# Kernel tuning notes

Measured on AMD Instinct MI355X. Metric: run time of the kernel, lower is better.

The kernel has to match this reference:

```python
import jax, jax.numpy as jnp
import numpy as np
import math

NUM_HEADS = 16
ROPE_BASE = 10000.0

def _rotate_half(t):
    d = t.shape[-1]
    x1, x2 = t[..., : d // 2], t[..., d // 2 :]
    return jnp.concatenate([-x2, x1], axis=-1)

def _rope_tables(seq_len, head_dim, dtype):
    inv_freq = 1.0 / (ROPE_BASE ** (jnp.arange(0, head_dim, 2, dtype=jnp.float32) / head_dim))
    t = jnp.arange(seq_len, dtype=jnp.float32)
    freqs = jnp.einsum('i,j->ij', t, inv_freq)          # [S, d/2]
    emb = jnp.concatenate([freqs, freqs], axis=-1)      # [S, d]
    return jnp.cos(emb).astype(dtype), jnp.sin(emb).astype(dtype)

def setup_inputs() -> dict:
    key = jax.random.key(0)
    ks = jax.random.split(key, 6)
    B, S, HID = 4, 2048, 1024
    x = jax.random.normal(ks[0], (B, S, HID), dtype=jnp.float32)
    w_scale = 0.02
    Wq = jax.random.normal(ks[1], (HID, HID), dtype=jnp.float32) * w_scale
    Wk = jax.random.normal(ks[2], (HID, HID), dtype=jnp.float32) * w_scale
    Wv = jax.random.normal(ks[3], (HID, HID), dtype=jnp.float32) * w_scale
    Wo = jax.random.normal(ks[4], (HID, HID), dtype=jnp.float32) * w_scale
    # ragged valid lengths in [S//2, S] so each sequence is non-trivial
    seq_lens = jax.random.randint(ks[5], (B,), S // 2, S + 1, dtype=jnp.int32)
    return {"x": x, "Wq": Wq, "Wk": Wk, "Wv": Wv, "Wo": Wo, "seq_lens": seq_lens}

def reference(x, Wq, Wk, Wv, Wo, seq_lens):
    B, S, HID = x.shape
    H = NUM_HEADS
    d = HID // H
    scale = 1.0 / math.sqrt(d)

    # qkv projections (nn.Linear, no bias)
    q = (x @ Wq).reshape(B, S, H, d)
    k = (x @ Wk).reshape(B, S, H, d)
    v = (x @ Wv).reshape(B, S, H, d)

    # fused RoPE, positions start at 0 for every sequence (prefill, beg=0)
    cos, sin = _rope_tables(S, d, x.dtype)              # [S, d]
    cos = cos[None, :, None, :]
    sin = sin[None, :, None, :]
    q = q * cos + _rotate_half(q) * sin
    k = k * cos + _rotate_half(k) * sin

    # causal SDPA over ragged batch via padding masks
    scores = jnp.einsum('bqhd,bkhd->bhqk', q, k) * scale  # [B,H,S,S]
    pos = jnp.arange(S)
    causal = pos[:, None] >= pos[None, :]                 # [S,S]
    valid_k = pos[None, :] < seq_lens[:, None]            # [B,S]
    mask = causal[None, None, :, :] & valid_k[:, None, None, :]
    neg = jnp.asarray(-1e9, dtype=scores.dtype)
    attn = jax.nn.softmax(jnp.where(mask, scores, neg), axis=-1)
    out = jnp.einsum('bhqk,bkhd->bqhd', attn, v).reshape(B, S, HID)

    out = out @ Wo
    # zero out padded query positions (they do not exist in CatTensor)
    valid_q = (pos[None, :] < seq_lens[:, None])[..., None]
    return jnp.where(valid_q, out, jnp.zeros((), dtype=out.dtype))
```

## Files before the change

### kernel.cpp

```cpp
#include <hip/hip_runtime.h>
#include <hip/hip_bf16.h>

typedef __attribute__((ext_vector_type(8))) short short8;
typedef __attribute__((ext_vector_type(4))) float f32x4;

constexpr int Bc   = 4;
constexpr int Sc   = 2048;
constexpr int HIDc = 1024;
constexpr int Hc   = 16;
constexpr size_t FB = (size_t)Bc * Sc * HIDc;
constexpr size_t WN = (size_t)HIDc * HIDc;
constexpr size_t TB = (size_t)Sc * 32;

__device__ __forceinline__ int get_L(const int* seq, int b)
{
    return (seq[1] == 0) ? seq[2 * b] : seq[b];
}

__device__ __forceinline__ short f2bf(float v)
{
    __hip_bfloat16 h = __float2bfloat16(v);
    return *reinterpret_cast<short*>(&h);
}
__device__ __forceinline__ float bf2f(short s)
{
    __hip_bfloat16 h = *reinterpret_cast<__hip_bfloat16*>(&s);
    return __bfloat162float(h);
}
__device__ __forceinline__ unsigned pack2(short a, short b)
{
    return (unsigned)(unsigned short)a | ((unsigned)(unsigned short)b << 16);
}

__global__ __launch_bounds__(256) void rope_tab(float* __restrict__ ct,
                                                float* __restrict__ st)
{
    const int idx = blockIdx.x * 256 + threadIdx.x;
    const int s = idx >> 5;
    const int j = idx & 31;
    const float ang = (float)s * powf(10000.0f, -(float)j * (1.0f / 32.0f));
    ct[idx] = cosf(ang);
    st[idx] = sinf(ang);
}

__global__ __launch_bounds__(256) void split_pass(const float* __restrict__ in,
                                                  short* __restrict__ hi,
                                                  short* __restrict__ lo)
{
    const size_t i8 = ((size_t)blockIdx.x * 256 + threadIdx.x) * 8;
    const float4 u0 = *(const float4*)(in + i8);
    const float4 u1 = *(const float4*)(in + i8 + 4);
    const float v[8] = {u0.x, u0.y, u0.z, u0.w, u1.x, u1.y, u1.z, u1.w};
    short8 h, l;
#pragma unroll
    for (int j = 0; j < 8; j++) {
        const short hb = f2bf(v[j]);
        h[j] = hb;
        l[j] = f2bf(v[j] - bf2f(hb));
    }
    *(short8*)(hi + i8) = h;
    *(short8*)(lo + i8) = l;
}

__global__ __launch_bounds__(256) void rope_split(const float* __restrict__ p,
                                                  short* __restrict__ hi,
                                                  short* __restrict__ lo)
{
    const int idx = blockIdx.x * 256 + threadIdx.x;
    const int jc = idx & 3;
    const int h  = (idx >> 2) & 15;
    const int s  = (idx >> 6) & 2047;
    const int b  = idx >> 17;
    const int j0 = jc * 8;
    const size_t base = ((size_t)(b * Sc + s)) * HIDc + h * 64 + j0;

    const float4 a0 = *(const float4*)(p + base);
    const float4 a1 = *(const float4*)(p + base + 4);
    const float4 b0 = *(const float4*)(p + base + 32);
    const float4 b1 = *(const float4*)(p + base + 36);
    const float x1[8] = {a0.x, a0.y, a0.z, a0.w, a1.x, a1.y, a1.z, a1.w};
    const float x2[8] = {b0.x, b0.y, b0.z, b0.w, b1.x, b1.y, b1.z, b1.w};

    short8 h1, h2, l1, l2;
#pragma unroll
    for (int jj = 0; jj < 8; jj++) {
        const int j = j0 + jj;
        const float ang = (float)s * powf(10000.0f, -(float)j * (1.0f / 32.0f));
        const float cv = cosf(ang);
        const float sv = sinf(ang);
        const float y1 = x1[jj] * cv - x2[jj] * sv;
        const float y2 = x2[jj] * cv + x1[jj] * sv;
        const short hb1 = f2bf(y1), hb2 = f2bf(y2);
        h1[jj] = hb1; l1[jj] = f2bf(y1 - bf2f(hb1));
        h2[jj] = hb2; l2[jj] = f2bf(y2 - bf2f(hb2));
    }
    *(short8*)(hi + base)      = h1;
    *(short8*)(hi + base + 32) = h2;
    *(short8*)(lo + base)      = l1;
    *(short8*)(lo + base + 32) = l2;
}

__global__ __launch_bounds__(256) void vsplit_t(const float* __restrict__ V,
                                                short* __restrict__ th,
                                                short* __restrict__ tl)
{
    __shared__ float T[64][65];
    const int s0 = blockIdx.x * 64;
    const int h  = blockIdx.y & 15;
    const int b  = blockIdx.y >> 4;
    const int t  = threadIdx.x;
    const int r  = t >> 2;
    const int c  = (t & 3) * 16;
#pragma unroll
    for (int j = 0; j < 4; j++) {
        const float4 u = *(const float4*)(V + ((size_t)(b * Sc + s0 + r)) * HIDc + h * 64 + c + j * 4);
        T[r][c + j * 4 + 0] = u.x; T[r][c + j * 4 + 1] = u.y;
        T[r][c + j * 4 + 2] = u.z; T[r][c + j * 4 + 3] = u.w;
    }
    __syncthreads();
    short8 h0, h1, l0, l1;
#pragma unroll
    for (int j = 0; j < 8; j++) {
        const float v = T[c + j][r];
        const short hb = f2bf(v);
        h0[j] = hb; l0[j] = f2bf(v - bf2f(hb));
    }
#pragma unroll
    for (int j = 0; j < 8; j++) {
        const float v = T[c + 8 + j][r];
        const short hb = f2bf(v);
        h1[j] = hb; l1[j] = f2bf(v - bf2f(hb));
    }
    const size_t dst = ((size_t)(b * Hc + h) * 64 + r) * Sc + s0 + c;
    *(short8*)(th + dst)     = h0;
    *(short8*)(th + dst + 8) = h1;
    *(short8*)(tl + dst)     = l0;
    *(short8*)(tl + dst + 8) = l1;
}

__device__ __forceinline__ void wsplit_body(const float* __restrict__ W,
                                            short* __restrict__ th,
                                            short* __restrict__ tl,
                                            float (*T)[65])
{
    const int t  = threadIdx.x;
    const int n0 = blockIdx.x * 64;
    const int k0 = blockIdx.y * 64;
    const int r  = t >> 2;
    const int c  = (t & 3) * 16;
#pragma unroll
    for (int j = 0; j < 4; j++) {
        const float4 u = *(const float4*)(W + (size_t)(k0 + r) * HIDc + n0 + c + j * 4);
        T[r][c + j * 4 + 0] = u.x; T[r][c + j * 4 + 1] = u.y;
        T[r][c + j * 4 + 2] = u.z; T[r][c + j * 4 + 3] = u.w;
    }
    __syncthreads();
    short8 h0, h1, l0, l1;
#pragma unroll
    for (int j = 0; j < 8; j++) {
        const float v = T[c + j][r];
        const short hb = f2bf(v);
        h0[j] = hb; l0[j] = f2bf(v - bf2f(hb));
    }
#pragma unroll
    for (int j = 0; j < 8; j++) {
        const float v = T[c + 8 + j][r];
        const short hb = f2bf(v);
        h1[j] = hb; l1[j] = f2bf(v - bf2f(hb));
    }
    const size_t dst = (size_t)(n0 + r) * HIDc + k0 + c;
    *(short8*)(th + dst)     = h0;
    *(short8*)(th + dst + 8) = h1;
    *(short8*)(tl + dst)     = l0;
    *(short8*)(tl + dst + 8) = l1;
}

__global__ __launch_bounds__(256) void wsplit_t(const float* __restrict__ W,
                                                short* __restrict__ th,
                                                short* __restrict__ tl)
{
    __shared__ float T[64][65];
    wsplit_body(W, th, tl, T);
}

__global__ __launch_bounds__(256) void wsplit4_t(
    const float* __restrict__ W0, const float* __restrict__ W1,
    const float* __restrict__ W2, const float* __restrict__ W3,
    short* __restrict__ out)
{
    __shared__ float T[64][65];
    const int z = blockIdx.z;
    const float* W = (z == 0) ? W0 : (z == 1) ? W1 : (z == 2) ? W2 : W3;
    short* th = out + (size_t)z * 2 * WN;
    wsplit_body(W, th, th + WN, T);
}

__device__ __forceinline__ void gemm_x3_acc(
    const short* __restrict__ Ah, const short* __restrict__ Al,
    const short* __restrict__ Bh, const short* __restrict__ Bl,
    const int m0, const int n0,
    short* AhS, short* AlS, short* BhS, short* BlS,
    f32x4 (&acc)[4][4])
{
    const int t    = threadIdx.x;
    const int lane = t & 63;
    const int wid  = t >> 6;
    const int wr   = (wid >> 1) * 64;
    const int wc   = (wid & 1) * 64;
    const int lr   = lane & 15;
    const int lg   = lane >> 4;

#pragma unroll
    for (int mi = 0; mi < 4; mi++)
#pragma unroll
        for (int ni = 0; ni < 4; ni++) acc[mi][ni] = (f32x4)(0.f);

    for (int k0 = 0; k0 < HIDc; k0 += 64) {
        __syncthreads();
#pragma unroll
        for (int i = 0; i < 4; i++) {
            const int o  = i * 4096 + t * 16;
            const int r  = o >> 7;
            const int sc = (o & 127) ^ ((r & 7) << 4);
            const int k  = sc >> 1;
            const size_t ga = (size_t)(m0 + r) * HIDc + k0 + k;
            const size_t gb = (size_t)(n0 + r) * HIDc + k0 + k;
            __builtin_amdgcn_global_load_lds(
                (const __attribute__((address_space(1))) void*)(Ah + ga),
                (__attribute__((address_space(3))) void*)(AhS + (o >> 1)), 16, 0, 0);
            __builtin_amdgcn_global_load_lds(
                (const __attribute__((address_space(1))) void*)(Al + ga),
                (__attribute__((address_space(3))) void*)(AlS + (o >> 1)), 16, 0, 0);
            __builtin_amdgcn_global_load_lds(
                (const __attribute__((address_space(1))) void*)(Bh + gb),
                (__attribute__((address_space(3))) void*)(BhS + (o >> 1)), 16, 0, 0);
            __builtin_amdgcn_global_load_lds(
                (const __attribute__((address_space(1))) void*)(Bl + gb),
                (__attribute__((address_space(3))) void*)(BlS + (o >> 1)), 16, 0, 0);
        }
        __syncthreads();

        short8 a_h[4][2], a_l[4][2];
#pragma unroll
        for (int mi = 0; mi < 4; mi++) {
            const int r = wr + mi * 16 + lr;
#pragma unroll
            for (int kk = 0; kk < 2; kk++) {
                const int cb  = kk * 64 + lg * 16;
                const int off = r * 128 + (cb ^ ((r & 7) << 4));
                a_h[mi][kk] = *(const short8*)((const char*)AhS + off);
                a_l[mi][kk] = *(const short8*)((const char*)AlS + off);
            }
        }
#pragma unroll
        for (int ni = 0; ni < 4; ni++) {
            const int rn = wc + ni * 16 + lr;
            short8 b_h[2], b_l[2];
#pragma unroll
            for (int kk = 0; kk < 2; kk++) {
                const int cb  = kk * 64 + lg * 16;
                const int off = rn * 128 + (cb ^ ((rn & 7) << 4));
                b_h[kk] = *(const short8*)((const char*)BhS + off);
                b_l[kk] = *(const short8*)((const char*)BlS + off);
            }
#pragma unroll
            for (int mi = 0; mi < 4; mi++) {
#pragma unroll
                for (int kk = 0; kk < 2; kk++) {
                    acc[mi][ni] = __builtin_amdgcn_mfma_f32_16x16x32_bf16(
                        a_h[mi][kk], b_h[kk], acc[mi][ni], 0, 0, 0);
                    acc[mi][ni] = __builtin_amdgcn_mfma_f32_16x16x32_bf16(
                        a_h[mi][kk], b_l[kk], acc[mi][ni], 0, 0, 0);
                    acc[mi][ni] = __builtin_amdgcn_mfma_f32_16x16x32_bf16(
                        a_l[mi][kk], b_h[kk], acc[mi][ni], 0, 0, 0);
                }
            }
        }
    }
}

__global__ __launch_bounds__(256, 2) void gemm_x3(
    const short* __restrict__ Ah, const short* __restrict__ Al,
    const short* __restrict__ Bh, const short* __restrict__ Bl,
    float* __restrict__ C, const int* __restrict__ seq)
{
    __shared__ alignas(16) short AhS[128 * 64];
    __shared__ alignas(16) short AlS[128 * 64];
    __shared__ alignas(16) short BhS[128 * 64];
    __shared__ alignas(16) short BlS[128 * 64];
    const int F   = blockIdx.x + 8 * blockIdx.y;
    const int xcd = F & 7;
    const int s   = F >> 3;
    const int ly  = xcd + 8 * (s >> 3);
    const int lx  = s & 7;
    const int m0 = ly * 128, n0 = lx * 128;

    f32x4 acc[4][4];
    gemm_x3_acc(Ah, Al, Bh, Bl, m0, n0, AhS, AlS, BhS, BlS, acc);

    const int lane = threadIdx.x & 63;
    const int wid  = threadIdx.x >> 6;
    const int wr   = (wid >> 1) * 64;
    const int wc   = (wid & 1) * 64;
    const int lr   = lane & 15;
    const int lg   = lane >> 4;
#pragma unroll
    for (int mi = 0; mi < 4; mi++) {
#pragma unroll
        for (int rr = 0; rr < 4; rr++) {
            const int row = m0 + wr + mi * 16 + lg * 4 + rr;
            bool zero = false;
            if (seq != nullptr) zero = ((row & 2047) >= get_L(seq, row >> 11));
#pragma unroll
            for (int ni = 0; ni < 4; ni++) {
                const float v = zero ? 0.f : acc[mi][ni][rr];
                C[(size_t)row * HIDc + n0 + wc + ni * 16 + lr] = v;
            }
        }
    }
}

__global__ __launch_bounds__(256, 2) void gemm_x3_qkv_rope(
    const short* __restrict__ Ah, const short* __restrict__ Al,
    const short* __restrict__ Wbase, short* __restrict__ outS,
    float* __restrict__ outF,
    const float* __restrict__ cos_t, const float* __restrict__ sin_t)
{
    __shared__ alignas(16) short AhS[128 * 64];
    __shared__ alignas(16) short AlS[128 * 64];
    __shared__ alignas(16) short BhS[128 * 64];
    __shared__ alignas(16) short BlS[128 * 64];
    const int F   = blockIdx.x + 8 * blockIdx.y + 512 * blockIdx.z;
    const int xcd = F & 7;
    const int s   = F >> 3;
    const int ly  = xcd + 8 * (s / 24);
    const int rem = s % 24;
    const int lx  = rem & 7;
    const int lz  = rem >> 3;
    const int m0 = ly * 128, n0 = lx * 128;
    const short* Bh = Wbase + (size_t)lz * 2 * WN;

    f32x4 acc[4][4];
    gemm_x3_acc(Ah, Al, Bh, Bh + WN, m0, n0, AhS, AlS, BhS, BlS, acc);

    const int lane = threadIdx.x & 63;
    const int wid  = threadIdx.x >> 6;
    const int wr   = (wid >> 1) * 64;
    const int wc   = (wid & 1) * 64;
    const int lr   = lane & 15;
    const int lg   = lane >> 4;

    if (lz < 2) {
        short* Ch = outS + (size_t)lz * 2 * FB;
        short* Cl = Ch + FB;
#pragma unroll
        for (int mi = 0; mi < 4; mi++) {
#pragma unroll
            for (int rr = 0; rr < 4; rr++) {
                const int row = m0 + wr + mi * 16 + lg * 4 + rr;
                const int sp  = row & 2047;
                const float c0  = cos_t[sp * 32 + lr];
                const float sn0 = sin_t[sp * 32 + lr];
                const float c1  = cos_t[sp * 32 + 16 + lr];
                const float sn1 = sin_t[sp * 32 + 16 + lr];
                const float x0 = acc[mi][0][rr];
                const float x1 = acc[mi][1][rr];
                const float x2 = acc[mi][2][rr];
                const float x3 = acc[mi][3][rr];
                const float y[4] = {x0 * c0 - x2 * sn0,
                                    x1 * c1 - x3 * sn1,
                                    x2 * c0 + x0 * sn0,
                                    x3 * c1 + x1 * sn1};
                const size_t cb = (size_t)row * HIDc + n0 + wc + lr;
#pragma unroll
                for (int ni = 0; ni < 4; ni++) {
                    const short hb = f2bf(y[ni]);
                    Ch[cb + ni * 16] = hb;
                    Cl[cb + ni * 16] = f2bf(y[ni] - bf2f(hb));
                }
            }
        }
    } else {
#pragma unroll
        for (int mi = 0; mi < 4; mi++) {
#pragma unroll
            for (int rr = 0; rr < 4; rr++) {
                const int row = m0 + wr + mi * 16 + lg * 4 + rr;
#pragma unroll
                for (int ni = 0; ni < 4; ni++)
                    outF[(size_t)row * HIDc + n0 + wc + ni * 16 + lr] = acc[mi][ni][rr];
            }
        }
    }
}

__global__ __launch_bounds__(256, 3) void attn_mfma_sw(
    const short* __restrict__ Qh, const short* __restrict__ Ql,
    const short* __restrict__ Kh, const short* __restrict__ Kl,
    const short* __restrict__ Vth, const short* __restrict__ Vtl,
    short* __restrict__ Oh, short* __restrict__ Ol,
    const int* __restrict__ seq)
{
    __shared__ alignas(16) short KhS[64 * 64];
    __shared__ alignas(16) short KlS[64 * 64];
    __shared__ alignas(16) short VhS[64 * 64];
    __shared__ alignas(16) short VlS[64 * 64];
    __shared__ alignas(16) short PhS[4][16 * 64];
    __shared__ alignas(16) short PlS[4][16 * 64];

    const int blk  = blockIdx.x;
    const int bh   = blk & 63;
    const int qt   = 31 - (blk >> 6);
    const int h    = bh & 15;
    const int b    = bh >> 4;
    const int q0   = qt * 64;
    const int L    = get_L(seq, b);
    const int t    = threadIdx.x;
    const int w    = t >> 6;
    const int lane = t & 63;
    const int lr   = lane & 15;
    const int lg   = lane >> 4;

    if (q0 >= L) {
        const int r = t >> 2;
        const int c = (t & 3) * 16;
        const size_t base = ((size_t)(b * Sc + q0 + r)) * HIDc + h * 64 + c;
        const short8 z = {0, 0, 0, 0, 0, 0, 0, 0};
        *(short8*)(Oh + base)     = z;
        *(short8*)(Oh + base + 8) = z;
        *(short8*)(Ol + base)     = z;
        *(short8*)(Ol + base + 8) = z;
        return;
    }

    short8 qb_h[2], qb_l[2];
    {
        const size_t qrow = ((size_t)(b * Sc + q0 + w * 16 + lr)) * HIDc + h * 64;
        qb_h[0] = *(const short8*)(Qh + qrow + lg * 8);
        qb_h[1] = *(const short8*)(Qh + qrow + 32 + lg * 8);
        qb_l[0] = *(const short8*)(Ql + qrow + lg * 8);
        qb_l[1] = *(const short8*)(Ql + qrow + 32 + lg * 8);
    }

    f32x4 oacc[4];
#pragma unroll
    for (int t2 = 0; t2 < 4; t2++) oacc[t2] = (f32x4)(0.f);
    float m_s = -1.0e30f, l_s = 0.f;

    const int qpos = q0 + w * 16 + lr;

    const int kend = min(q0 + 64, L);
    for (int kb = 0; kb < kend; kb += 64) {
        __syncthreads();
#pragma unroll
        for (int i = 0; i < 2; i++) {
            const int o  = i * 4096 + t * 16;
            const int r  = o >> 7;
            const int sc = (o & 127) ^ ((r & 7) << 4);
            const int k  = sc >> 1;
            const size_t gk = ((size_t)(b * Sc + kb + r)) * HIDc + h * 64 + k;
            const size_t gv = ((size_t)(b * Hc + h) * 64 + r) * Sc + kb + k;
            __builtin_amdgcn_global_load_lds(
                (const __attribute__((address_space(1))) void*)(Kh + gk),
                (__attribute__((address_space(3))) void*)((char*)KhS + o), 16, 0, 0);
            __builtin_amdgcn_global_load_lds(
                (const __attribute__((address_space(1))) void*)(Kl + gk),
                (__attribute__((address_space(3))) void*)((char*)KlS + o), 16, 0, 0);
            __builtin_amdgcn_global_load_lds(
                (const __attribute__((address_space(1))) void*)(Vth + gv),
                (__attribute__((address_space(3))) void*)((char*)VhS + o), 16, 0, 0);
            __builtin_amdgcn_global_load_lds(
                (const __attribute__((address_space(1))) void*)(Vtl + gv),
                (__attribute__((address_space(3))) void*)((char*)VlS + o), 16, 0, 0);
        }
        __syncthreads();

        f32x4 s4[4];
#pragma unroll
        for (int tt = 0; tt < 4; tt++) s4[tt] = (f32x4)(0.f);
        __builtin_amdgcn_s_setprio(1);
#pragma unroll
        for (int tt = 0; tt < 4; tt++) {
            const int rn = tt * 16 + lr;
#pragma unroll
            for (int kk = 0; kk < 2; kk++) {
                const int off = rn * 128 + ((kk * 64 + lg * 16) ^ ((rn & 7) << 4));
                const short8 ka_h = *(const short8*)((const char*)KhS + off);
                const short8 ka_l = *(const short8*)((const char*)KlS + off);
                s4[tt] = __builtin_amdgcn_mfma_f32_16x16x32_bf16(ka_h, qb_h[kk], s4[tt], 0, 0, 0);
                s4[tt] = __builtin_amdgcn_mfma_f32_16x16x32_bf16(ka_h, qb_l[kk], s4[tt], 0, 0, 0);
                s4[tt] = __builtin_amdgcn_mfma_f32_16x16x32_bf16(ka_l, qb_h[kk], s4[tt], 0, 0, 0);
            }
        }
        __builtin_amdgcn_s_setprio(0);

        float tmax = -1.0e30f;
#pragma unroll
        for (int tt = 0; tt < 4; tt++)
#pragma unroll
            for (int r = 0; r < 4; r++) {
                const int kpos = kb + tt * 16 + lg * 4 + r;
                const bool valid = (kpos <= qpos) && (kpos < L);
                const float v = valid ? s4[tt][r] * 0.125f : -1.0e9f;
                s4[tt][r] = v;
                tmax = fmaxf(tmax, v);
            }
        tmax = fmaxf(tmax, __shfl_xor(tmax, 16));
        tmax = fmaxf(tmax, __shfl_xor(tmax, 32));
        const float mnew  = fmaxf(m_s, tmax);
        const float alpha = __expf(m_s - mnew);
        float psum = 0.f;
#pragma unroll
        for (int tt = 0; tt < 4; tt++)
#pragma unroll
            for (int r = 0; r < 4; r++) {
                const float e = __expf(s4[tt][r] - mnew);
                s4[tt][r] = e;
                psum += e;
            }
        psum += __shfl_xor(psum, 16);
        psum += __shfl_xor(psum, 32);
        l_s = alpha * l_s + psum;
        m_s = mnew;

#pragma unroll
        for (int r = 0; r < 4; r++) {
            const float ar = __shfl(alpha, lg * 4 + r);
#pragma unroll
            for (int t2 = 0; t2 < 4; t2++) oacc[t2][r] *= ar;
        }

#pragma unroll
        for (int tt = 0; tt < 4; tt++) {
            const short h0 = f2bf(s4[tt][0]); const short l0 = f2bf(s4[tt][0] - bf2f(h0));
            const short h1 = f2bf(s4[tt][1]); const short l1 = f2bf(s4[tt][1] - bf2f(h1));
            const short h2 = f2bf(s4[tt][2]); const short l2 = f2bf(s4[tt][2] - bf2f(h2));
            const short h3 = f2bf(s4[tt][3]); const short l3 = f2bf(s4[tt][3] - bf2f(h3));
            const int off = lr * 128 + ((tt * 32 + lg * 8) ^ ((lr & 7) << 4));
            uint2 uh; uh.x = pack2(h0, h1); uh.y = pack2(h2, h3);
            uint2 ul; ul.x = pack2(l0, l1); ul.y = pack2(l2, l3);
            *(uint2*)((char*)&PhS[w][0] + off) = uh;
            *(uint2*)((char*)&PlS[w][0] + off) = ul;
        }

        __builtin_amdgcn_sched_barrier(0);

        short8 pa_h[2], pa_l[2];
#pragma unroll
        for (int kk = 0; kk < 2; kk++) {
            const int poff = lr * 128 + ((kk * 64 + lg * 16) ^ ((lr & 7) << 4));
            pa_h[kk] = *(const short8*)((const char*)&PhS[w][0] + poff);
            pa_l[kk] = *(const short8*)((const char*)&PlS[w][0] + poff);
        }
        __builtin_amdgcn_s_setprio(1);
#pragma unroll
        for (int t2 = 0; t2 < 4; t2++) {
            const int rv = t2 * 16 + lr;
#pragma unroll
            for (int kk = 0; kk < 2; kk++) {
                const int voff = rv * 128 + ((kk * 64 + lg * 16) ^ ((rv & 7) << 4));
                const short8 vb_h = *(const short8*)((const char*)VhS + voff);
                const short8 vb_l = *(const short8*)((const char*)VlS + voff);
                oacc[t2] = __builtin_amdgcn_mfma_f32_16x16x32_bf16(pa_h[kk], vb_h, oacc[t2], 0, 0, 0);
                oacc[t2] = __builtin_amdgcn_mfma_f32_16x16x32_bf16(pa_h[kk], vb_l, oacc[t2], 0, 0, 0);
                oacc[t2] = __builtin_amdgcn_mfma_f32_16x16x32_bf16(pa_l[kk], vb_h, oacc[t2], 0, 0, 0);
            }
        }
        __builtin_amdgcn_s_setprio(0);
    }

#pragma unroll
    for (int r = 0; r < 4; r++) {
        const float lrow = __shfl(l_s, lg * 4 + r);
        const float inv  = 1.0f / lrow;
        const int   row  = q0 + w * 16 + lg * 4 + r;
        const size_t base = ((size_t)(b * Sc + row)) * HIDc + h * 64;
#pragma unroll
        for (int t2 = 0; t2 < 4; t2++) {
            const float v = oacc[t2][r] * inv;
            const short hb = f2bf(v);
            Oh[base + t2 * 16 + lr] = hb;
            Ol[base + t2 * 16 + lr] = f2bf(v - bf2f(hb));
        }
    }
}

__global__ __launch_bounds__(256) void gemm64(
    const float* __restrict__ A, const float* __restrict__ W,
    float* __restrict__ C, const int K, const int N,
    const int* __restrict__ seq)
{
    __shared__ float As[32][68];
    __shared__ float Bs[32][68];

    const int t  = threadIdx.x;
    const int m0 = blockIdx.y * 64;
    const int n0 = blockIdx.x * 64;
    const int ty = t >> 4, tx = t & 15;
    const int ar = t >> 2;
    const int ac = (t & 3) * 8;
    const int wr = t >> 3;
    const int wc = (t & 7) * 8;

    float acc[4][4];
#pragma unroll
    for (int i = 0; i < 4; i++)
#pragma unroll
        for (int j = 0; j < 4; j++) acc[i][j] = 0.f;

    for (int k0 = 0; k0 < K; k0 += 32) {
        __syncthreads();
        {
            const float* p = A + (size_t)(m0 + ar) * K + k0 + ac;
            const float4 u0 = *(const float4*)p;
            const float4 u1 = *(const float4*)(p + 4);
            As[ac + 0][ar] = u0.x; As[ac + 1][ar] = u0.y;
            As[ac + 2][ar] = u0.z; As[ac + 3][ar] = u0.w;
            As[ac + 4][ar] = u1.x; As[ac + 5][ar] = u1.y;
            As[ac + 6][ar] = u1.z; As[ac + 7][ar] = u1.w;
        }
        {
            const float* p = W + (size_t)(k0 + wr) * N + n0 + wc;
            const float4 u0 = *(const float4*)p;
            const float4 u1 = *(const float4*)(p + 4);
            *(float4*)&Bs[wr][wc]     = u0;
            *(float4*)&Bs[wr][wc + 4] = u1;
        }
        __syncthreads();

#pragma unroll 8
        for (int kk = 0; kk < 32; kk++) {
            const float4 a4 = *(const float4*)&As[kk][ty * 4];
            const float4 b4 = *(const float4*)&Bs[kk][tx * 4];
            const float av[4] = {a4.x, a4.y, a4.z, a4.w};
            const float bv[4] = {b4.x, b4.y, b4.z, b4.w};
#pragma unroll
            for (int i = 0; i < 4; i++)
#pragma unroll
                for (int j = 0; j < 4; j++)
                    acc[i][j] = fmaf(av[i], bv[j], acc[i][j]);
        }
    }

#pragma unroll
    for (int i = 0; i < 4; i++) {
        const int row = m0 + ty * 4 + i;
        bool zero = false;
        if (seq != nullptr) zero = ((row & 2047) >= get_L(seq, row >> 11));
#pragma unroll
        for (int j = 0; j < 4; j++) {
            const float v = zero ? 0.f : acc[i][j];
            C[(size_t)row * N + n0 + tx * 4 + j] = v;
        }
    }
}

__global__ __launch_bounds__(256) void rope_pair(float* __restrict__ p)
{
    const int idx = blockIdx.x * 256 + threadIdx.x;
    const int j = idx & 31;
    const int h = (idx >> 5) & 15;
    const int s = (idx >> 9) & 2047;
    const int b = idx >> 20;
    const size_t base = ((size_t)(b * Sc + s)) * HIDc + h * 64 + j;

    const float x1 = p[base];
    const float x2 = p[base + 32];
    const float ang = (float)s * powf(10000.0f, -(float)j * (1.0f / 32.0f));
    const float cv = cosf(ang);
    const float sv = sinf(ang);
    p[base]      = x1 * cv - x2 * sv;
    p[base + 32] = x2 * cv + x1 * sv;
}

__device__ __forceinline__ int swz(int r, int chunk)
{
    return (((chunk ^ (r >> 2)) & 15) << 2);
}

__global__ __launch_bounds__(256) void attn64(
    const float* Q, const float* __restrict__ K,
    const float* __restrict__ V, float* O,
    const int* __restrict__ seq)
{
    __shared__ float Qs[64][64];
    __shared__ float Ks[64][64];
    __shared__ float Vs[64][64];

    const int blk = blockIdx.x;
    const int bh  = blk & 63;
    const int qt  = 31 - (blk >> 6);
    const int h   = bh & 15;
    const int b   = bh >> 4;
    const int q0  = qt * 64;
    const int L   = get_L(seq, b);
    const int t   = threadIdx.x;
    const int qg  = t >> 4;
    const int kg  = t & 15;

    if (q0 >= L) {
#pragma unroll
        for (int i = 0; i < 4; i++) {
            const size_t row = (size_t)(b * Sc + q0 + qg * 4 + i);
#pragma unroll
            for (int c = 0; c < 4; c++)
                O[row * HIDc + h * 64 + kg * 4 + c] = 0.f;
        }
        return;
    }

    {
        const int r = t >> 2;
        const int c = (t & 3) * 16;
        const float* src = Q + ((size_t)(b * Sc + q0 + r)) * HIDc + h * 64 + c;
#pragma unroll
        for (int jj = 0; jj < 4; jj++)
            *(float4*)&Qs[r][swz(r, (c >> 2) + jj)] = *(const float4*)(src + 4 * jj);
    }

    float m_i[4], l_i[4], acc[4][4];
#pragma unroll
    for (int i = 0; i < 4; i++) {
        m_i[i] = -1.0e30f; l_i[i] = 0.f;
#pragma unroll
        for (int c = 0; c < 4; c++) acc[i][c] = 0.f;
    }

    const int kend = min(q0 + 64, L);
    for (int kb = 0; kb < kend; kb += 64) {
        __syncthreads();
        {
            const int r = t >> 2;
            const int c = (t & 3) * 16;
            const size_t off = ((size_t)(b * Sc + kb + r)) * HIDc + h * 64 + c;
#pragma unroll
            for (int jj = 0; jj < 4; jj++)
                *(float4*)&Ks[r][swz(r, (c >> 2) + jj)] = *(const float4*)(K + off + 4 * jj);
#pragma unroll
            for (int jj = 0; jj < 4; jj++)
                *(float4*)&Vs[r][swz(r, (c >> 2) + jj)] = *(const float4*)(V + off + 4 * jj);
        }
        __syncthreads();

        float s[4][4];
#pragma unroll
        for (int i = 0; i < 4; i++)
#pragma unroll
            for (int c = 0; c < 4; c++) s[i][c] = 0.f;

#pragma unroll 4
        for (int dc = 0; dc < 64; dc += 4) {
            float4 q4[4], k4[4];
#pragma unroll
            for (int i = 0; i < 4; i++)
                q4[i] = *(const float4*)&Qs[qg * 4 + i][swz(qg * 4 + i, dc >> 2)];
#pragma unroll
            for (int c = 0; c < 4; c++)
                k4[c] = *(const float4*)&Ks[kg * 4 + c][swz(kg * 4 + c, dc >> 2)];
#pragma unroll
            for (int i = 0; i < 4; i++)
#pragma unroll
                for (int c = 0; c < 4; c++) {
                    s[i][c] = fmaf(q4[i].x, k4[c].x, s[i][c]);
                    s[i][c] = fmaf(q4[i].y, k4[c].y, s[i][c]);
                    s[i][c] = fmaf(q4[i].z, k4[c].z, s[i][c]);
                    s[i][c] = fmaf(q4[i].w, k4[c].w, s[i][c]);
                }
        }

#pragma unroll
        for (int i = 0; i < 4; i++) {
            const int qpos = q0 + qg * 4 + i;
#pragma unroll
            for (int c = 0; c < 4; c++) {
                const int kpos = kb + kg * 4 + c;
                const bool valid = (kpos <= qpos) && (kpos < L);
                s[i][c] = valid ? s[i][c] * 0.125f : -1.0e9f;
            }
        }

#pragma unroll
        for (int i = 0; i < 4; i++) {
            float tm = fmaxf(fmaxf(s[i][0], s[i][1]), fmaxf(s[i][2], s[i][3]));
#pragma unroll
            for (int off = 1; off < 16; off <<= 1)
                tm = fmaxf(tm, __shfl_xor(tm, off));
            const float mnew  = fmaxf(m_i[i], tm);
            const float alpha = __expf(m_i[i] - mnew);

            float psum = 0.f;
#pragma unroll
            for (int c = 0; c < 4; c++) {
                s[i][c] = __expf(s[i][c] - mnew);
                psum += s[i][c];
            }
#pragma unroll
            for (int off = 1; off < 16; off <<= 1)
                psum += __shfl_xor(psum, off);

            l_i[i] = alpha * l_i[i] + psum;
            m_i[i] = mnew;
#pragma unroll
            for (int c = 0; c < 4; c++) acc[i][c] *= alpha;
        }

        __syncthreads();
#pragma unroll
        for (int i = 0; i < 4; i++)
#pragma unroll
            for (int c = 0; c < 4; c++) {
                const int pr = kg * 4 + c;
                Ks[pr][swz(pr, qg) + i] = s[i][c];
            }
        __syncthreads();

#pragma unroll 4
        for (int ki = 0; ki < 64; ki++) {
            const float4 p4 = *(const float4*)&Ks[ki][swz(ki, qg)];
            const float4 v4 = *(const float4*)&Vs[ki][swz(ki, kg)];
            const float pv[4] = {p4.x, p4.y, p4.z, p4.w};
            const float vv[4] = {v4.x, v4.y, v4.z, v4.w};
#pragma unroll
            for (int i = 0; i < 4; i++)
#pragma unroll
                for (int c = 0; c < 4; c++)
                    acc[i][c] = fmaf(pv[i], vv[c], acc[i][c]);
        }
    }

#pragma unroll
    for (int i = 0; i < 4; i++) {
        const float inv = 1.0f / l_i[i];
        const size_t row = (size_t)(b * Sc + q0 + qg * 4 + i);
#pragma unroll
        for (int c = 0; c < 4; c++)
            O[row * HIDc + h * 64 + kg * 4 + c] = acc[i][c] * inv;
    }
}

extern "C" void kernel_launch(void* const* d_in, const int* in_sizes, int n_in,
                              void* d_out, int out_size, void* d_ws, size_t ws_size,
                              hipStream_t stream)
{
    const float* x   = (const float*)d_in[0];
    const float* Wq  = (const float*)d_in[1];
    const float* Wk  = (const float*)d_in[2];
    const float* Wv  = (const float*)d_in[3];
    const float* Wo  = (const float*)d_in[4];
    const int*   seq = (const int*)d_in[5];

    const size_t needX3 = 3 * FB * sizeof(float) + 2 * WN * sizeof(short);
    const size_t needX4 = 3 * FB * sizeof(float) + 8 * WN * sizeof(short);
    const size_t needX5 = needX4 + 2 * TB * sizeof(float);

    const dim3 gg(HIDc / 128, Bc * Sc / 128);
    const int  sb  = (int)(FB / (8 * 256));
    const int  rsb = (int)(FB / (16 * 256));

    if (ws_size >= needX5) {
        short* ws_s = (short*)d_ws;
        short* W4   = ws_s + 6 * FB;
        float* cosT = (float*)(ws_s + 6 * FB + 8 * WN);
        float* sinT = cosT + TB;

        short* xh = (short*)d_out;
        short* xl = xh + FB;

        rope_tab<<<(int)(TB / 256), 256, 0, stream>>>(cosT, sinT);
        split_pass<<<sb, 256, 0, stream>>>(x, xh, xl);
        wsplit4_t<<<dim3(16, 16, 4), 256, 0, stream>>>(Wq, Wk, Wv, Wo, W4);

        float* Vf = (float*)(ws_s + 4 * FB);
        gemm_x3_qkv_rope<<<dim3(8, 64, 3), 256, 0, stream>>>(
            xh, xl, W4, ws_s, Vf, cosT, sinT);

        short* Vth = (short*)d_out;
        short* Vtl = Vth + FB;
        vsplit_t<<<dim3(32, 64), 256, 0, stream>>>(Vf, Vth, Vtl);

        short* Qh2 = ws_s;
        short* Ql2 = Qh2 + FB;
        short* Kh2 = ws_s + 2 * FB;
        short* Kl2 = Kh2 + FB;
        short* Oh2 = ws_s + 4 * FB;
        short* Ol2 = Oh2 + FB;
        attn_mfma_sw<<<Bc * Hc * (Sc / 64), 256, 0, stream>>>(
            Qh2, Ql2, Kh2, Kl2, Vth, Vtl, Oh2, Ol2, seq);

        gemm_x3<<<gg, 256, 0, stream>>>(Oh2, Ol2, W4 + 6 * WN, W4 + 7 * WN,
                                        (float*)d_out, seq);
    } else if (ws_size >= needX4) {
        float* Qf = (float*)d_ws;
        float* Kf = Qf + FB;
        float* Vf = Kf + FB;
        short* ws_s = (short*)d_ws;
        short* W4 = ws_s + 6 * FB;

        short* xh = (short*)d_out;
        short* xl = xh + FB;

        split_pass<<<sb, 256, 0, stream>>>(x, xh, xl);
        wsplit4_t<<<dim3(16, 16, 4), 256, 0, stream>>>(Wq, Wk, Wv, Wo, W4);
        {
            gemm_x3<<<gg, 256, 0, stream>>>(xh, xl, W4 + 0 * WN, W4 + 1 * WN, Qf, nullptr);
            gemm_x3<<<gg, 256, 0, stream>>>(xh, xl, W4 + 2 * WN, W4 + 3 * WN, Kf, nullptr);
            gemm_x3<<<gg, 256, 0, stream>>>(xh, xl, W4 + 4 * WN, W4 + 5 * WN, Vf, nullptr);
        }

        short* Qh2 = (short*)d_out;
        short* Ql2 = Qh2 + FB;
        rope_split<<<rsb, 256, 0, stream>>>(Qf, Qh2, Ql2);
        short* Kh2 = ws_s;
        short* Kl2 = Kh2 + FB;
        rope_split<<<rsb, 256, 0, stream>>>(Kf, Kh2, Kl2);
        short* Vth = ws_s + 2 * FB;
        short* Vtl = Vth + FB;
        vsplit_t<<<dim3(32, 64), 256, 0, stream>>>(Vf, Vth, Vtl);

        short* Oh2 = ws_s + 4 * FB;
        short* Ol2 = Oh2 + FB;
        attn_mfma_sw<<<Bc * Hc * (Sc / 64), 256, 0, stream>>>(
            Qh2, Ql2, Kh2, Kl2, Vth, Vtl, Oh2, Ol2, seq);

        gemm_x3<<<gg, 256, 0, stream>>>(Oh2, Ol2, W4 + 6 * WN, W4 + 7 * WN,
                                        (float*)d_out, seq);
    } else if (ws_size >= needX3) {
        float* Qf = (float*)d_ws;
        float* Kf = Qf + FB;
        float* Vf = Kf + FB;
        short* ws_s = (short*)d_ws;
        short* wh = ws_s + 6 * FB;
        short* wl = wh + WN;

        short* xh = (short*)d_out;
        short* xl = xh + FB;

        const dim3 wg(16, 16);

        split_pass<<<sb, 256, 0, stream>>>(x, xh, xl);

        wsplit_t<<<wg, 256, 0, stream>>>(Wq, wh, wl);
        gemm_x3<<<gg, 256, 0, stream>>>(xh, xl, wh, wl, Qf, nullptr);
        wsplit_t<<<wg, 256, 0, stream>>>(Wk, wh, wl);
        gemm_x3<<<gg, 256, 0, stream>>>(xh, xl, wh, wl, Kf, nullptr);
        wsplit_t<<<wg, 256, 0, stream>>>(Wv, wh, wl);
        gemm_x3<<<gg, 256, 0, stream>>>(xh, xl, wh, wl, Vf, nullptr);

        short* Qh2 = (short*)d_out;
        short* Ql2 = Qh2 + FB;
        rope_split<<<rsb, 256, 0, stream>>>(Qf, Qh2, Ql2);
        short* Kh2 = ws_s;
        short* Kl2 = Kh2 + FB;
        rope_split<<<rsb, 256, 0, stream>>>(Kf, Kh2, Kl2);
        short* Vth = ws_s + 2 * FB;
        short* Vtl = Vth + FB;
        vsplit_t<<<dim3(32, 64), 256, 0, stream>>>(Vf, Vth, Vtl);

        short* Oh2 = ws_s + 4 * FB;
        short* Ol2 = Oh2 + FB;
        attn_mfma_sw<<<Bc * Hc * (Sc / 64), 256, 0, stream>>>(
            Qh2, Ql2, Kh2, Kl2, Vth, Vtl, Oh2, Ol2, seq);

        wsplit_t<<<wg, 256, 0, stream>>>(Wo, wh, wl);
        gemm_x3<<<gg, 256, 0, stream>>>(Oh2, Ol2, wh, wl, (float*)d_out, seq);
    } else if (ws_size >= 3 * FB * sizeof(float)) {
        float* Q = (float*)d_ws;
        float* K = Q + FB;
        float* V = K + FB;

        const dim3 g64(HIDc / 64, Bc * Sc / 64);
        gemm64<<<g64, 256, 0, stream>>>(x, Wq, Q, HIDc, HIDc, nullptr);
        gemm64<<<g64, 256, 0, stream>>>(x, Wk, K, HIDc, HIDc, nullptr);
        gemm64<<<g64, 256, 0, stream>>>(x, Wv, V, HIDc, HIDc, nullptr);

        const int rb = Bc * Sc * Hc * 32 / 256;
        rope_pair<<<rb, 256, 0, stream>>>(Q);
        rope_pair<<<rb, 256, 0, stream>>>(K);

        attn64<<<Bc * Hc * (Sc / 64), 256, 0, stream>>>(Q, K, V, Q, seq);

        gemm64<<<g64, 256, 0, stream>>>(Q, Wo, (float*)d_out, HIDc, HIDc, seq);
    } else {
        hipMemsetAsync(d_out, 0, (size_t)out_size * sizeof(float), stream);
    }
}
```

Baseline: 379.4 us.

## Fuse V transpose and bf16 split into QKV GEMM epilogue

The V slice of the fused QKV GEMM no longer writes fp32 V to workspace for a separate vsplit_t kernel. It stages the accumulator tile in shared memory, transposes it, and writes the hi/lo bf16 transposed V directly with 16-byte stores. Workspace buffers are reassigned so xh/xl live in workspace and O reuses them. This removes one kernel launch and a full fp32 round-trip of V, at the cost of extra shared-memory syncs in the epilogue.

```diff
diff --git a/kernel.cpp b/kernel.cpp
--- a/kernel.cpp
+++ b/kernel.cpp
@@ -323,13 +323,10 @@
 __global__ __launch_bounds__(256, 2) void gemm_x3_qkv_rope(
     const short* __restrict__ Ah, const short* __restrict__ Al,
     const short* __restrict__ Wbase, short* __restrict__ outS,
-    float* __restrict__ outF,
+    short* __restrict__ Vth, short* __restrict__ Vtl,
     const float* __restrict__ cos_t, const float* __restrict__ sin_t)
 {
-    __shared__ alignas(16) short AhS[128 * 64];
-    __shared__ alignas(16) short AlS[128 * 64];
-    __shared__ alignas(16) short BhS[128 * 64];
-    __shared__ alignas(16) short BlS[128 * 64];
+    __shared__ alignas(16) short SB[4 * 128 * 64];
     const int F   = blockIdx.x + 8 * blockIdx.y + 512 * blockIdx.z;
     const int xcd = F & 7;
     const int s   = F >> 3;
@@ -341,10 +338,12 @@
     const short* Bh = Wbase + (size_t)lz * 2 * WN;
 
     f32x4 acc[4][4];
-    gemm_x3_acc(Ah, Al, Bh, Bh + WN, m0, n0, AhS, AlS, BhS, BlS, acc);
-
-    const int lane = threadIdx.x & 63;
-    const int wid  = threadIdx.x >> 6;
+    gemm_x3_acc(Ah, Al, Bh, Bh + WN, m0, n0,
+                SB, SB + 8192, SB + 16384, SB + 24576, acc);
+
+    const int t    = threadIdx.x;
+    const int lane = t & 63;
+    const int wid  = t >> 6;
     const int wr   = (wid >> 1) * 64;
     const int wc   = (wid & 1) * 64;
     const int lr   = lane & 15;
@@ -381,15 +380,39 @@
             }
         }
     } else {
-#pragma unroll
-        for (int mi = 0; mi < 4; mi++) {
+        float* TT = (float*)SB;
+        __syncthreads();
+#pragma unroll
+        for (int mi = 0; mi < 4; mi++)
 #pragma unroll
             for (int rr = 0; rr < 4; rr++) {
-                const int row = m0 + wr + mi * 16 + lg * 4 + rr;
+                const int row_l = wr + mi * 16 + lg * 4 + rr;
 #pragma unroll
                 for (int ni = 0; ni < 4; ni++)
-                    outF[(size_t)row * HIDc + n0 + wc + ni * 16 + lr] = acc[mi][ni][rr];
-            }
+                    TT[row_l * 128 + wc + ni * 16 + lr] = acc[mi][ni][rr];
+            }
+        __syncthreads();
+
+        const int bb = m0 >> 11;
+        const int s_base = m0 & 2047;
+        const int cl = t & 127;
+        const int sh = (t >> 7) * 64;
+        const int col = n0 + cl;
+        const int hh2 = col >> 6;
+        const int dd  = col & 63;
+        const size_t vbase = ((size_t)(bb * Hc + hh2) * 64 + dd) * Sc + s_base + sh;
+#pragma unroll
+        for (int j0 = 0; j0 < 64; j0 += 8) {
+            short8 hv, lv;
+#pragma unroll
+            for (int j = 0; j < 8; j++) {
+                const float v = TT[(sh + j0 + j) * 128 + cl];
+                const short hb = f2bf(v);
+                hv[j] = hb;
+                lv[j] = f2bf(v - bf2f(hb));
+            }
+            *(short8*)(Vth + vbase + j0) = hv;
+            *(short8*)(Vtl + vbase + j0) = lv;
         }
     }
 }
@@ -859,31 +882,28 @@
 
     if (ws_size >= needX5) {
         short* ws_s = (short*)d_ws;
+        short* Qh2  = ws_s;
+        short* Ql2  = Qh2 + FB;
+        short* Kh2  = ws_s + 2 * FB;
+        short* Kl2  = Kh2 + FB;
+        short* xh   = ws_s + 4 * FB;
+        short* xl   = xh + FB;
         short* W4   = ws_s + 6 * FB;
         float* cosT = (float*)(ws_s + 6 * FB + 8 * WN);
         float* sinT = cosT + TB;
 
-        short* xh = (short*)d_out;
-        short* xl = xh + FB;
+        short* Vth = (short*)d_out;
+        short* Vtl = Vth + FB;
 
         rope_tab<<<(int)(TB / 256), 256, 0, stream>>>(cosT, sinT);
         split_pass<<<sb, 256, 0, stream>>>(x, xh, xl);
         wsplit4_t<<<dim3(16, 16, 4), 256, 0, stream>>>(Wq, Wk, Wv, Wo, W4);
 
-        float* Vf = (float*)(ws_s + 4 * FB);
         gemm_x3_qkv_rope<<<dim3(8, 64, 3), 256, 0, stream>>>(
-            xh, xl, W4, ws_s, Vf, cosT, sinT);
-
-        short* Vth = (short*)d_out;
-        short* Vtl = Vth + FB;
-        vsplit_t<<<dim3(32, 64), 256, 0, stream>>>(Vf, Vth, Vtl);
-
-        short* Qh2 = ws_s;
-        short* Ql2 = Qh2 + FB;
-        short* Kh2 = ws_s + 2 * FB;
-        short* Kl2 = Kh2 + FB;
-        short* Oh2 = ws_s + 4 * FB;
-        short* Ol2 = Oh2 + FB;
+            xh, xl, W4, ws_s, Vth, Vtl, cosT, sinT);
+
+        short* Oh2 = xh;
+        short* Ol2 = xl;
         attn_mfma_sw<<<Bc * Hc * (Sc / 64), 256, 0, stream>>>(
             Qh2, Ql2, Kh2, Kl2, Vth, Vtl, Oh2, Ol2, seq);
 
@@ -901,11 +921,9 @@
 
         split_pass<<<sb, 256, 0, stream>>>(x, xh, xl);
         wsplit4_t<<<dim3(16, 16, 4), 256, 0, stream>>>(Wq, Wk, Wv, Wo, W4);
-        {
-            gemm_x3<<<gg, 256, 0, stream>>>(xh, xl, W4 + 0 * WN, W4 + 1 * WN, Qf, nullptr);
-            gemm_x3<<<gg, 256, 0, stream>>>(xh, xl, W4 + 2 * WN, W4 + 3 * WN, Kf, nullptr);
-            gemm_x3<<<gg, 256, 0, stream>>>(xh, xl, W4 + 4 * WN, W4 + 5 * WN, Vf, nullptr);
-        }
+        gemm_x3<<<gg, 256, 0, stream>>>(xh, xl, W4 + 0 * WN, W4 + 1 * WN, Qf, nullptr);
+        gemm_x3<<<gg, 256, 0, stream>>>(xh, xl, W4 + 2 * WN, W4 + 3 * WN, Kf, nullptr);
+        gemm_x3<<<gg, 256, 0, stream>>>(xh, xl, W4 + 4 * WN, W4 + 5 * WN, Vf, nullptr);
 
         short* Qh2 = (short*)d_out;
         short* Ql2 = Qh2 + FB;
```

New measurement: 358.8 us. 5.4% less time.
